# Kernel optimization log

Measured on AMD Instinct MI355X. Metric: run time of the kernel, lower is better.

The kernel has to match this reference:

```python
import jax, jax.numpy as jnp
import numpy as np

_USER_BASIS = [(0, 1), (2, 1), (4, 1), (8, 1), (1, 1), (6, 1), (10, 1), (12, 1),
               (3, -1), (5, -1), (9, -1), (14, 1), (7, 1), (11, 1), (13, 1), (15, -1)]
_MASK_TO_IDX = {mask: idx for idx, (mask, _) in enumerate(_USER_BASIS)}


def _blade_sign_pga(mask_a, mask_b):
    sign = 1
    for bit in range(4):
        if mask_a >> bit & 1:
            lower = mask_b & ((1 << bit) - 1)
            if bin(lower).count('1') % 2 == 1:
                sign = -sign
    return sign


def _build_pga_cayley_table():
    # table[k, i, j] = coeff of basis_k in basis_i * basis_j; values in {-1,0,+1}
    table = np.zeros((16, 16, 16), dtype=np.float32)
    for i, (mask_i, sign_i) in enumerate(_USER_BASIS):
        for j, (mask_j, sign_j) in enumerate(_USER_BASIS):
            if mask_i & mask_j & 1:  # shared null e0 -> product vanishes
                continue
            result_mask = mask_i ^ mask_j
            anticomm = _blade_sign_pga(mask_i, mask_j)
            k = _MASK_TO_IDX[result_mask]
            _, sign_k = _USER_BASIS[k]
            table[k, i, j] = float(sign_i * sign_j * anticomm * sign_k)
    return table


def setup_inputs() -> dict:
    key = jax.random.key(0)
    k1, k2 = jax.random.split(key)
    shape = (4, 4096, 128, 16)
    mv_a = jax.random.normal(k1, shape, dtype=jnp.float32)
    mv_b = jax.random.normal(k2, shape, dtype=jnp.float32)
    cayley = jnp.asarray(_build_pga_cayley_table())  # (16,16,16) buffer
    return {"mv_a": mv_a, "mv_b": mv_b, "cayley": cayley}


def reference(mv_a, mv_b, cayley):
    # Geometric product C[..., k] = sum_ij A[..., i] B[..., j] cayley[k, i, j]
    return jnp.einsum('...i,...j,kij->...k', mv_a, mv_b, cayley)
```

## Files before the change

kernel.cpp:

```cpp
#include <hip/hip_runtime.h>


namespace {

struct CayleyLUT {
    int idx[16][16];
    int sgn[16][16];
};

constexpr CayleyLUT make_lut() {
    CayleyLUT L{};
    constexpr int MASK[16] = {0, 2, 4, 8, 1, 6, 10, 12, 3, 5, 9, 14, 7, 11, 13, 15};
    constexpr int SIGN[16] = {1, 1, 1, 1, 1, 1, 1, 1, -1, -1, -1, 1, 1, 1, 1, -1};
    for (int i = 0; i < 16; ++i) {
        for (int j = 0; j < 16; ++j) {
            L.idx[i][j] = 0;
            L.sgn[i][j] = 0;
            if (MASK[i] & MASK[j] & 1) continue;
            const int rm = MASK[i] ^ MASK[j];
            int k = 0;
            for (int t = 0; t < 16; ++t)
                if (MASK[t] == rm) k = t;
            int s = 1;
            for (int bit = 0; bit < 4; ++bit) {
                if ((MASK[i] >> bit) & 1) {
                    int lower = MASK[j] & ((1 << bit) - 1);
                    int c = 0;
                    for (int x = lower; x; x >>= 1) c += x & 1;
                    if (c & 1) s = -s;
                }
            }
            L.idx[i][j] = k;
            L.sgn[i][j] = SIGN[i] * SIGN[j] * s * SIGN[k];
        }
    }
    return L;
}

constexpr CayleyLUT LUT = make_lut();

__device__ __forceinline__ int slot(int m, int q) {
    return m * 16 + ((q ^ ((m >> 1) & 3)) << 2);
}

__device__ __forceinline__ void gp_compute(const float* a, const float* b, float* c) {
#pragma unroll
    for (int k = 0; k < 16; ++k) c[k] = 0.0f;
#pragma unroll
    for (int i = 0; i < 16; ++i) {
#pragma unroll
        for (int j = 0; j < 16; ++j) {
            const int s = LUT.sgn[i][j];
            if (s != 0) {
                const int k = LUT.idx[i][j];
                c[k] = fmaf(s > 0 ? a[i] : -a[i], b[j], c[k]);
            }
        }
    }
}

__global__ __launch_bounds__(256) void gp_kernel(const float* __restrict__ A,
                                                 const float* __restrict__ B,
                                                 float* __restrict__ C,
                                                 long long n_mv) {
    __shared__ float sA[256 * 16];
    __shared__ float sB[256 * 16];
    const int t = threadIdx.x;
    const long long base_mv = (long long)blockIdx.x * 256;
    const bool full = (base_mv + 256 <= n_mv);
    const int mv_here = full ? 256 : (int)(n_mv - base_mv);
    const int nf4 = mv_here * 4;

    const float4* __restrict__ A4 = reinterpret_cast<const float4*>(A) + base_mv * 4;
    const float4* __restrict__ B4 = reinterpret_cast<const float4*>(B) + base_mv * 4;
    float4* __restrict__ C4 = reinterpret_cast<float4*>(C) + base_mv * 4;

    if (full) {
#pragma unroll
        for (int r = 0; r < 4; ++r) {
            const int f = t + 256 * r;
            const float4 va = A4[f];
            const float4 vb = B4[f];
            const int o = slot(f >> 2, f & 3);
            *reinterpret_cast<float4*>(&sA[o]) = va;
            *reinterpret_cast<float4*>(&sB[o]) = vb;
        }
    } else {
#pragma unroll
        for (int r = 0; r < 4; ++r) {
            const int f = t + 256 * r;
            if (f < nf4) {
                const float4 va = A4[f];
                const float4 vb = B4[f];
                const int o = slot(f >> 2, f & 3);
                *reinterpret_cast<float4*>(&sA[o]) = va;
                *reinterpret_cast<float4*>(&sB[o]) = vb;
            }
        }
    }
    __syncthreads();

    if (full || t < mv_here) {
        float a[16], b[16];
#pragma unroll
        for (int q = 0; q < 4; ++q) {
            const int o = slot(t, q);
            const float4 va = *reinterpret_cast<const float4*>(&sA[o]);
            const float4 vb = *reinterpret_cast<const float4*>(&sB[o]);
            a[4 * q + 0] = va.x; a[4 * q + 1] = va.y; a[4 * q + 2] = va.z; a[4 * q + 3] = va.w;
            b[4 * q + 0] = vb.x; b[4 * q + 1] = vb.y; b[4 * q + 2] = vb.z; b[4 * q + 3] = vb.w;
        }
        float c[16];
        gp_compute(a, b, c);
#pragma unroll
        for (int q = 0; q < 4; ++q) {
            float4 v;
            v.x = c[4 * q + 0]; v.y = c[4 * q + 1]; v.z = c[4 * q + 2]; v.w = c[4 * q + 3];
            *reinterpret_cast<float4*>(&sA[slot(t, q)]) = v;
        }
    }
    __syncthreads();

    if (full) {
#pragma unroll
        for (int r = 0; r < 4; ++r) {
            const int f = t + 256 * r;
            C4[f] = *reinterpret_cast<const float4*>(&sA[slot(f >> 2, f & 3)]);
        }
    } else {
#pragma unroll
        for (int r = 0; r < 4; ++r) {
            const int f = t + 256 * r;
            if (f < nf4) {
                C4[f] = *reinterpret_cast<const float4*>(&sA[slot(f >> 2, f & 3)]);
            }
        }
    }
}

}

extern "C" void kernel_launch(void* const* d_in, const int* in_sizes, int n_in,
                              void* d_out, int out_size, void* d_ws, size_t ws_size,
                              hipStream_t stream) {
    const float* A = (const float*)d_in[0];
    const float* B = (const float*)d_in[1];
    float* C = (float*)d_out;
    const long long n_mv = (long long)in_sizes[0] / 16;
    const int nblocks = (int)((n_mv + 255) / 256);
    gp_kernel<<<nblocks, 256, 0, stream>>>(A, B, C, n_mv);
}
```

Measured before the change: 76.93 us.

## Use per-wave LDS staging and drop block barriers, storing output directly

Each 64-lane wave now stages its own slice of A and B in a private shared-memory region, so the two block-wide barriers are removed. Results are written to global memory directly from registers instead of round-tripping through LDS for a coalesced store. This cuts synchronisation and LDS traffic, but the direct stores have a 64-byte lane stride, and the code relies on the implicit in-order execution of a wave for LDS visibility.

```diff
diff --git a/kernel.cpp b/kernel.cpp
--- a/kernel.cpp
+++ b/kernel.cpp
@@ -63,50 +63,38 @@
                                                  const float* __restrict__ B,
                                                  float* __restrict__ C,
                                                  long long n_mv) {
-    __shared__ float sA[256 * 16];
-    __shared__ float sB[256 * 16];
-    const int t = threadIdx.x;
-    const long long base_mv = (long long)blockIdx.x * 256;
-    const bool full = (base_mv + 256 <= n_mv);
-    const int mv_here = full ? 256 : (int)(n_mv - base_mv);
-    const int nf4 = mv_here * 4;
+    __shared__ float sA[4][64 * 16];
+    __shared__ float sB[4][64 * 16];
+    const int tid = threadIdx.x;
+    const int wid = tid >> 6;
+    const int lane = tid & 63;
+    float* __restrict__ wA = sA[wid];
+    float* __restrict__ wB = sB[wid];
 
-    const float4* __restrict__ A4 = reinterpret_cast<const float4*>(A) + base_mv * 4;
-    const float4* __restrict__ B4 = reinterpret_cast<const float4*>(B) + base_mv * 4;
-    float4* __restrict__ C4 = reinterpret_cast<float4*>(C) + base_mv * 4;
+    const long long wave_mv = (long long)blockIdx.x * 256 + (long long)(wid << 6);
+    if (wave_mv >= n_mv) return;
+    const long long rem = n_mv - wave_mv;
 
-    if (full) {
+    const float4* __restrict__ A4 = reinterpret_cast<const float4*>(A) + (wave_mv << 2);
+    const float4* __restrict__ B4 = reinterpret_cast<const float4*>(B) + (wave_mv << 2);
+    float4* __restrict__ C4 = reinterpret_cast<float4*>(C) + (wave_mv << 2);
+
+    if (rem >= 64) {
 #pragma unroll
         for (int r = 0; r < 4; ++r) {
-            const int f = t + 256 * r;
+            const int f = (r << 6) + lane;
             const float4 va = A4[f];
             const float4 vb = B4[f];
             const int o = slot(f >> 2, f & 3);
-            *reinterpret_cast<float4*>(&sA[o]) = va;
-            *reinterpret_cast<float4*>(&sB[o]) = vb;
+            *reinterpret_cast<float4*>(&wA[o]) = va;
+            *reinterpret_cast<float4*>(&wB[o]) = vb;
         }
-    } else {
-#pragma unroll
-        for (int r = 0; r < 4; ++r) {
-            const int f = t + 256 * r;
-            if (f < nf4) {
-                const float4 va = A4[f];
-                const float4 vb = B4[f];
-                const int o = slot(f >> 2, f & 3);
-                *reinterpret_cast<float4*>(&sA[o]) = va;
-                *reinterpret_cast<float4*>(&sB[o]) = vb;
-            }
-        }
-    }
-    __syncthreads();
-
-    if (full || t < mv_here) {
         float a[16], b[16];
 #pragma unroll
         for (int q = 0; q < 4; ++q) {
-            const int o = slot(t, q);
-            const float4 va = *reinterpret_cast<const float4*>(&sA[o]);
-            const float4 vb = *reinterpret_cast<const float4*>(&sB[o]);
+            const int o = slot(lane, q);
+            const float4 va = *reinterpret_cast<const float4*>(&wA[o]);
+            const float4 vb = *reinterpret_cast<const float4*>(&wB[o]);
             a[4 * q + 0] = va.x; a[4 * q + 1] = va.y; a[4 * q + 2] = va.z; a[4 * q + 3] = va.w;
             b[4 * q + 0] = vb.x; b[4 * q + 1] = vb.y; b[4 * q + 2] = vb.z; b[4 * q + 3] = vb.w;
         }
@@ -116,23 +104,38 @@
         for (int q = 0; q < 4; ++q) {
             float4 v;
             v.x = c[4 * q + 0]; v.y = c[4 * q + 1]; v.z = c[4 * q + 2]; v.w = c[4 * q + 3];
-            *reinterpret_cast<float4*>(&sA[slot(t, q)]) = v;
+            C4[(lane << 2) + q] = v;
         }
-    }
-    __syncthreads();
-
-    if (full) {
+    } else {
+        const int nf4 = (int)(rem << 2);
 #pragma unroll
         for (int r = 0; r < 4; ++r) {
-            const int f = t + 256 * r;
-            C4[f] = *reinterpret_cast<const float4*>(&sA[slot(f >> 2, f & 3)]);
+            const int f = (r << 6) + lane;
+            if (f < nf4) {
+                const float4 va = A4[f];
+                const float4 vb = B4[f];
+                const int o = slot(f >> 2, f & 3);
+                *reinterpret_cast<float4*>(&wA[o]) = va;
+                *reinterpret_cast<float4*>(&wB[o]) = vb;
+            }
         }
-    } else {
+        if (lane < (int)rem) {
+            float a[16], b[16];
 #pragma unroll
-        for (int r = 0; r < 4; ++r) {
-            const int f = t + 256 * r;
-            if (f < nf4) {
-                C4[f] = *reinterpret_cast<const float4*>(&sA[slot(f >> 2, f & 3)]);
+            for (int q = 0; q < 4; ++q) {
+                const int o = slot(lane, q);
+                const float4 va = *reinterpret_cast<const float4*>(&wA[o]);
+                const float4 vb = *reinterpret_cast<const float4*>(&wB[o]);
+                a[4 * q + 0] = va.x; a[4 * q + 1] = va.y; a[4 * q + 2] = va.z; a[4 * q + 3] = va.w;
+                b[4 * q + 0] = vb.x; b[4 * q + 1] = vb.y; b[4 * q + 2] = vb.z; b[4 * q + 3] = vb.w;
+            }
+            float c[16];
+            gp_compute(a, b, c);
+#pragma unroll
+            for (int q = 0; q < 4; ++q) {
+                float4 v;
+                v.x = c[4 * q + 0]; v.y = c[4 * q + 1]; v.z = c[4 * q + 2]; v.w = c[4 * q + 3];
+                C4[(lane << 2) + q] = v;
             }
         }
     }
```

Measured after the change: 80.38 us. 4.5% more time.
